# Kernel optimization log

Hardware: AMD Instinct MI355X
Metric: run time of the kernel (lower is better)

The kernel has to match this reference:

```python
import jax, jax.numpy as jnp
import numpy as np
import math

NUM_HEADS = 8
D_HEAD = 128
DEPTH = 1
LAMBDA_INIT = 0.8 - 0.6 * math.exp(-0.3 * DEPTH)
EPS = 1e-5


def setup_inputs() -> dict:
    key = jax.random.key(0)
    ks = jax.random.split(key, 10)
    B, N, D = 2, 2048, 1024
    s = 0.02
    return {
        "X": jax.random.normal(ks[0], (B, N, D), jnp.float32),
        "Wq": jax.random.normal(ks[1], (2 * D_HEAD * NUM_HEADS, D), jnp.float32) * s,
        "Wk": jax.random.normal(ks[2], (2 * D_HEAD * NUM_HEADS, D), jnp.float32) * s,
        "Wv": jax.random.normal(ks[3], (2 * D_HEAD * NUM_HEADS, D), jnp.float32) * s,
        "Wo": jax.random.normal(ks[4], (D, 2 * D_HEAD * NUM_HEADS), jnp.float32) * s,
        "lambda_q1": jax.random.normal(ks[5], (NUM_HEADS, D_HEAD), jnp.float32) * 0.1,
        "lambda_k1": jax.random.normal(ks[6], (NUM_HEADS, D_HEAD), jnp.float32) * 0.1,
        "lambda_q2": jax.random.normal(ks[7], (NUM_HEADS, D_HEAD), jnp.float32) * 0.1,
        "lambda_k2": jax.random.normal(ks[8], (NUM_HEADS, D_HEAD), jnp.float32) * 0.1,
        "rms_scale": jnp.ones((2 * D_HEAD,), jnp.float32),
    }


def reference(X, Wq, Wk, Wv, Wo, lambda_q1, lambda_k1, lambda_q2, lambda_k2, rms_scale):
    B, N, D = X.shape
    H, dh = NUM_HEADS, D_HEAD

    def proj(W):
        # (B, N, 2*H*dh) -> (B, H, N, 2*dh)
        y = jnp.einsum('bnd,ed->bne', X, W)
        return y.reshape(B, N, H, 2 * dh).transpose(0, 2, 1, 3)

    Q = proj(Wq)
    K = proj(Wk)
    V = proj(Wv)
    Q1, Q2 = Q[..., :dh], Q[..., dh:]
    K1, K2 = K[..., :dh], K[..., dh:]

    lam1 = jnp.exp(jnp.sum(lambda_q1 * lambda_k1, axis=-1))  # (H,)
    lam2 = jnp.exp(jnp.sum(lambda_q2 * lambda_k2, axis=-1))
    lam = (lam1 - lam2 + LAMBDA_INIT)[None, :, None, None]  # (1, H, 1, 1)

    scaling = 1.0 / math.sqrt(dh)
    A1 = jnp.einsum('bhqd,bhkd->bhqk', Q1, K1) * scaling
    A2 = jnp.einsum('bhqd,bhkd->bhqk', Q2, K2) * scaling
    attn = jax.nn.softmax(A1, axis=-1) - lam * jax.nn.softmax(A2, axis=-1)

    O = jnp.einsum('bhqk,bhkd->bhqd', attn, V)  # (B, H, N, 2*dh)
    rms = jnp.sqrt(jnp.mean(O * O, axis=-1, keepdims=True) + EPS)
    O = O / rms * rms_scale
    O = O * (1.0 - LAMBDA_INIT)
    O = O.transpose(0, 2, 1, 3).reshape(B, N, H * 2 * dh)
    return jnp.einsum('bne,de->bnd', O, Wo)
```

## Files before the change

### kernel.cpp

```cpp
#include <hip/hip_runtime.h>
#include <hip/hip_bf16.h>

typedef __bf16 bf16;
typedef __attribute__((ext_vector_type(8))) __bf16 bf16x8;
typedef __attribute__((ext_vector_type(4))) float f32x4;

#define LAMBDA_INIT_F 0.3555090675909693f
#define RMS_EPS 1e-5f
#define QSCALE_F 0.1275174053237f

__device__ __forceinline__ void gl_lds16(const bf16* g, bf16* l) {
  __builtin_amdgcn_global_load_lds(
      (const __attribute__((address_space(1))) unsigned int*)g,
      (__attribute__((address_space(3))) unsigned int*)l, 16, 0, 0);
}
__device__ __forceinline__ void gl_lds4(const bf16* g, bf16* l) {
  __builtin_amdgcn_global_load_lds(
      (const __attribute__((address_space(1))) unsigned int*)g,
      (__attribute__((address_space(3))) unsigned int*)l, 4, 0, 0);
}

__global__ void fused_cast(const float* __restrict__ X, const float* __restrict__ Wq,
                           const float* __restrict__ Wk, const float* __restrict__ Wv,
                           const float* __restrict__ Wo, bf16* __restrict__ out) {
  constexpr int T4 = 3145728;
  int idx = blockIdx.x * blockDim.x + threadIdx.x;
  int stride = gridDim.x * blockDim.x;
  for (int i = idx; i < T4; i += stride) {
    const float* src;
    int off;
    if (i < 1048576)       { src = X;  off = i; }
    else if (i < 1572864)  { src = Wq; off = i - 1048576; }
    else if (i < 2097152)  { src = Wk; off = i - 1572864; }
    else if (i < 2621440)  { src = Wv; off = i - 2097152; }
    else                   { src = Wo; off = i - 2621440; }
    float4 v = reinterpret_cast<const float4*>(src)[off];
    bf16 o[4];
    o[0] = (bf16)v.x; o[1] = (bf16)v.y; o[2] = (bf16)v.z; o[3] = (bf16)v.w;
    *reinterpret_cast<ushort4*>(&out[(size_t)i * 4]) = *reinterpret_cast<const ushort4*>(o);
  }
}

template <int MODE, int BM>
__global__ __launch_bounds__(256) void gemm_bt(
    const bf16* __restrict__ A, const bf16* __restrict__ B,
    void* __restrict__ Cv, int M, int N, int K) {
  constexpr int BN = 128, BK = 32;
  constexpr int MF = BM / 32;
  constexpr int CA = BM / 16;
  __shared__ __align__(16) bf16 As[2][BM * BK];
  __shared__ __align__(16) bf16 Bs[2][BN * BK];
  const int tid = threadIdx.x, lane = tid & 63, w = tid >> 6;
  const int l15 = lane & 15, lhi = lane >> 4;
  const int wr = (w >> 1) * (BM / 2), wc = (w & 1) * 64;
  const int bm = blockIdx.x * BM, bn = blockIdx.y * BN;
  const int srow = lane >> 2, scol = (lane & 3) * 8;
  const int NTK = K / BK;
  f32x4 acc[MF][4] = {};

  auto stage = [&](int buf, int k0) {
#pragma unroll
    for (int i = 0; i < CA / 4; ++i) {
      int c = w * (CA / 4) + i;
      gl_lds16(&A[(size_t)(bm + c * 16 + srow) * K + k0 + scol], &As[buf][c * 512]);
    }
#pragma unroll
    for (int i = 0; i < 2; ++i) {
      int c = w * 2 + i;
      gl_lds16(&B[(size_t)(bn + c * 16 + srow) * K + k0 + scol], &Bs[buf][c * 512]);
    }
  };

  stage(0, 0);
  __syncthreads();
  for (int t = 0; t < NTK; ++t) {
    const int buf = t & 1;
    if (t + 1 < NTK) stage(buf ^ 1, (t + 1) * BK);
    bf16x8 af[MF], bfr[4];
#pragma unroll
    for (int mf = 0; mf < MF; ++mf)
      af[mf] = *reinterpret_cast<const bf16x8*>(&As[buf][(wr + mf * 16 + l15) * BK + lhi * 8]);
#pragma unroll
    for (int nf = 0; nf < 4; ++nf)
      bfr[nf] = *reinterpret_cast<const bf16x8*>(&Bs[buf][(wc + nf * 16 + l15) * BK + lhi * 8]);
#pragma unroll
    for (int mf = 0; mf < MF; ++mf)
#pragma unroll
      for (int nf = 0; nf < 4; ++nf)
        acc[mf][nf] = __builtin_amdgcn_mfma_f32_16x16x32_bf16(af[mf], bfr[nf], acc[mf][nf], 0, 0, 0);
    __syncthreads();
  }

#pragma unroll
  for (int mf = 0; mf < MF; ++mf)
#pragma unroll
    for (int nf = 0; nf < 4; ++nf)
#pragma unroll
      for (int r = 0; r < 4; ++r) {
        int m = bm + wr + mf * 16 + lhi * 4 + r;
        int n = bn + wc + nf * 16 + l15;
        if constexpr (MODE == 1) {
          ((float*)Cv)[(size_t)m * N + n] = acc[mf][nf][r];
        } else {
          int reg = n >> 11, nl = n & 2047;
          if (reg == 0) {
            ((bf16*)Cv)[(size_t)m * 2048 + nl] = (bf16)(acc[mf][nf][r] * QSCALE_F);
          } else if (reg == 1) {
            ((bf16*)Cv)[(size_t)(m + 4096) * 2048 + nl] = (bf16)acc[mf][nf][r];
          } else {
            int bb = m >> 11, nq = m & 2047;
            int hh = nl >> 8, e = nl & 255;
            ((bf16*)Cv)[(size_t)16777216 + ((((size_t)bb * 8 + hh) * 256 + e) << 11) + nq] =
                (bf16)acc[mf][nf][r];
          }
        }
      }
}

__global__ __launch_bounds__(512, 4) void diff_attn(
    const bf16* __restrict__ Q, const bf16* __restrict__ Kb, const bf16* __restrict__ Vtg,
    const float* __restrict__ lq1, const float* __restrict__ lk1,
    const float* __restrict__ lq2, const float* __restrict__ lk2,
    const float* __restrict__ rms_scale, bf16* __restrict__ Ob) {
  constexpr int NSEQ = 2048, E = 2048, KT = 32, NT = NSEQ / KT;
  __shared__ __align__(16) char smem[65536];
  float* Z = (float*)smem;

  const int tid = threadIdx.x, lane = tid & 63, w = tid >> 6;
  const int l15 = lane & 15, lhi = lane >> 4;
  const int g = w >> 1, s = w & 1;

  const int bid = blockIdx.x;
  const int orig = (bid & 7) * 64 + (bid >> 3);
  const int bh = orig >> 5;
  const int qb = orig & 31;
  const int b = bh >> 3, h = bh & 7;
  const int q0 = qb * 64;

  float lam = 0.f;
  if (s) {
    float sl1 = 0.f, sl2 = 0.f;
    for (int i = 0; i < 128; ++i) {
      sl1 += lq1[h * 128 + i] * lk1[h * 128 + i];
      sl2 += lq2[h * 128 + i] * lk2[h * 128 + i];
    }
    lam = __expf(sl1) - __expf(sl2) + LAMBDA_INIT_F;
  }

  const size_t qbase = ((size_t)b * NSEQ + q0 + g * 16 + l15) * E + (size_t)h * 256 + s * 128;
  bf16x8 qf[4];
#pragma unroll
  for (int df = 0; df < 4; ++df)
    qf[df] = *reinterpret_cast<const bf16x8*>(&Q[qbase + df * 32 + lhi * 8]);

  const bf16* Kbase = Kb + ((size_t)b * NSEQ) * E + (size_t)h * 256;
  const bf16* Vbase = Vtg + (((size_t)b * 8 + h) * 256) * (size_t)NSEQ;

  const int krow_sub = lane >> 5;
  const int kslot = lane & 31;
  const int ve_sub = lane >> 4;
  const int swz = l15 & 7;
  const int vq2 = (l15 >> 1) & 3;
  const int voff = (lhi ^ vq2) << 3;

  f32x4 o[16] = {};
  float ll = 0.f;

  auto stage = [&](int buf, int t) {
    const int kt0 = t * KT;
    bf16* Ksl = (bf16*)(smem + buf * 32768);
    bf16* Vsl = Ksl + 8192;
#pragma unroll
    for (int i = 0; i < 2; ++i) {
      int c = w * 2 + i;
      int row = 2 * c + krow_sub;
      gl_lds16(&Kbase[(size_t)(kt0 + row) * E + ((kslot ^ (row & 7)) << 3)], &Ksl[c * 512]);
    }
#pragma unroll
    for (int i = 0; i < 8; ++i) {
      int c = w * 8 + i;
      int r = 4 * c + ve_sub;
      int p = (lane & 15) ^ (((r >> 1) & 3) << 2);
      int key0 = 16 * ((p >> 1) & 1) + 4 * (p >> 2) + (p & 1) * 2;
      gl_lds4(&Vbase[(size_t)r * NSEQ + kt0 + key0], &Vsl[c * 128]);
    }
  };

  stage(0, 0);
  __syncthreads();

  for (int t = 0; t < NT; ++t) {
    const int buf = t & 1;
    const bf16* Ksl = (const bf16*)(smem + buf * 32768);
    const bf16* Vsl = Ksl + 8192;

    f32x4 sv0 = {}, sv1 = {};
#pragma unroll
    for (int df = 0; df < 4; ++df) {
      const int slot = (((s << 4) + df * 4 + lhi) ^ swz) << 3;
      bf16x8 kf0 = *reinterpret_cast<const bf16x8*>(&Ksl[l15 * 256 + slot]);
      bf16x8 kf1 = *reinterpret_cast<const bf16x8*>(&Ksl[(16 + l15) * 256 + slot]);
      sv0 = __builtin_amdgcn_mfma_f32_16x16x32_bf16(kf0, qf[df], sv0, 0, 0, 0);
      sv1 = __builtin_amdgcn_mfma_f32_16x16x32_bf16(kf1, qf[df], sv1, 0, 0, 0);
    }

    __builtin_amdgcn_sched_barrier(0);
    if (t + 1 < NT) stage(buf ^ 1, t + 1);
    __builtin_amdgcn_sched_barrier(0);

    bf16 pb[8];
    float rsum = 0.f;
#pragma unroll
    for (int r = 0; r < 4; ++r) {
      float e0 = __builtin_amdgcn_exp2f(sv0[r]);
      float e1 = __builtin_amdgcn_exp2f(sv1[r]);
      rsum += e0 + e1;
      pb[r] = (bf16)e0;
      pb[4 + r] = (bf16)e1;
    }
    ll += rsum;
    bf16x8 pa = *reinterpret_cast<const bf16x8*>(pb);

    __builtin_amdgcn_s_setprio(1);
#pragma unroll
    for (int eb = 0; eb < 16; ++eb) {
      bf16x8 vf = *reinterpret_cast<const bf16x8*>(&Vsl[(eb * 16 + l15) * 32 + voff]);
      o[eb] = __builtin_amdgcn_mfma_f32_16x16x32_bf16(pa, vf, o[eb], 0, 0, 0);
    }
    __builtin_amdgcn_s_setprio(0);

    __syncthreads();
  }

  ll += __shfl_xor(ll, 16, 64);
  ll += __shfl_xor(ll, 32, 64);
  float L[4];
#pragma unroll
  for (int r = 0; r < 4; ++r) L[r] = __shfl(ll, 4 * lhi + r, 64);

  if (s) {
    float* Zg = Z + g * 4096;
#pragma unroll
    for (int r = 0; r < 4; ++r) {
      float i2 = lam / L[r];
#pragma unroll
      for (int eb = 0; eb < 16; ++eb)
        Zg[(4 * lhi + r) * 256 + eb * 16 + l15] = o[eb][r] * i2;
    }
  }
  __syncthreads();
  if (!s) {
    const float osc = 1.0f - LAMBDA_INIT_F;
    const float* Zg = Z + g * 4096;
#pragma unroll
    for (int r = 0; r < 4; ++r) {
      float i1 = 1.0f / L[r];
      float vals[16];
      float ssq = 0.f;
#pragma unroll
      for (int eb = 0; eb < 16; ++eb) {
        float v = o[eb][r] * i1 - Zg[(4 * lhi + r) * 256 + eb * 16 + l15];
        vals[eb] = v;
        ssq += v * v;
      }
#pragma unroll
      for (int off = 1; off < 16; off <<= 1) ssq += __shfl_xor(ssq, off, 64);
      float rinv = rsqrtf(ssq * (1.0f / 256.0f) + RMS_EPS);
      const int q = q0 + g * 16 + 4 * lhi + r;
      const size_t ob = ((size_t)b * NSEQ + q) * E + (size_t)h * 256;
#pragma unroll
      for (int eb = 0; eb < 16; ++eb) {
        int e = eb * 16 + l15;
        Ob[ob + e] = (bf16)(vals[eb] * rinv * rms_scale[e] * osc);
      }
    }
  }
}

extern "C" void kernel_launch(void* const* d_in, const int* in_sizes, int n_in,
                              void* d_out, int out_size, void* d_ws, size_t ws_size,
                              hipStream_t stream) {
  const float* X   = (const float*)d_in[0];
  const float* Wq  = (const float*)d_in[1];
  const float* Wk  = (const float*)d_in[2];
  const float* Wv  = (const float*)d_in[3];
  const float* Wo  = (const float*)d_in[4];
  const float* lq1 = (const float*)d_in[5];
  const float* lk1 = (const float*)d_in[6];
  const float* lq2 = (const float*)d_in[7];
  const float* lk2 = (const float*)d_in[8];
  const float* rs  = (const float*)d_in[9];
  float* out = (float*)d_out;

  constexpr size_t B = 2, NSEQ = 2048, D = 1024, E = 2048;
  constexpr size_t M = B * NSEQ;

  char* ws = (char*)d_ws;
  bf16* Xb  = (bf16*)ws;
  bf16* Wqb = Xb + M * D;
  bf16* Wkb = Wqb + E * D;
  bf16* Wvb = Wkb + E * D;
  bf16* Wob = Wvb + E * D;
  bf16* Qb  = Wob + D * E;
  bf16* Kb  = Qb + M * E;
  bf16* Vtb = Kb + M * E;
  bf16* Ob  = Vtb + M * E;

  fused_cast<<<2048, 256, 0, stream>>>(X, Wq, Wk, Wv, Wo, Xb);

  gemm_bt<3, 128><<<dim3(M / 128, 6144 / 128), 256, 0, stream>>>(
      Xb, Wqb, Qb, (int)M, 6144, (int)D);

  diff_attn<<<dim3(512), 512, 0, stream>>>(Qb, Kb, Vtb, lq1, lk1, lq2, lk2, rs, Ob);

  gemm_bt<1, 64><<<dim3(M / 64, D / 128), 256, 0, stream>>>(Ob, Wob, out, (int)M, (int)D, (int)E);
}
```

Before: 275.3 us.

## Switch differential attention to 32x32x16 MFMA tiles with 128-query blocks

Rewrites the attention kernel around 32x32x16 bf16 MFMA instead of 16x16x32. Each block now covers 128 queries, so the grid halves and each K/V tile loaded into LDS is reused across more queries. V is now staged with 16-byte global-to-LDS loads, with K and V staging split across different waves. Probabilities are packed with v_cvt_pk_bf16_f32 and exchanged across lanes to form the operand, and the cross-wave Z buffer is stored as bf16. The rms_scale and output-scale multiply moves into the Wo bf16 cast. Costs and risks: register pressure is higher (launch bounds drop to 2 waves), there is extra shuffle work, and Z loses precision.

```diff
diff --git a/kernel.cpp b/kernel.cpp
--- a/kernel.cpp
+++ b/kernel.cpp
@@ -4,6 +4,8 @@
 typedef __bf16 bf16;
 typedef __attribute__((ext_vector_type(8))) __bf16 bf16x8;
 typedef __attribute__((ext_vector_type(4))) float f32x4;
+typedef __attribute__((ext_vector_type(16))) float f32x16;
+typedef __attribute__((ext_vector_type(4))) unsigned int u32x4;
 
 #define LAMBDA_INIT_F 0.3555090675909693f
 #define RMS_EPS 1e-5f
@@ -14,27 +16,30 @@
       (const __attribute__((address_space(1))) unsigned int*)g,
       (__attribute__((address_space(3))) unsigned int*)l, 16, 0, 0);
 }
-__device__ __forceinline__ void gl_lds4(const bf16* g, bf16* l) {
-  __builtin_amdgcn_global_load_lds(
-      (const __attribute__((address_space(1))) unsigned int*)g,
-      (__attribute__((address_space(3))) unsigned int*)l, 4, 0, 0);
-}
 
 __global__ void fused_cast(const float* __restrict__ X, const float* __restrict__ Wq,
                            const float* __restrict__ Wk, const float* __restrict__ Wv,
-                           const float* __restrict__ Wo, bf16* __restrict__ out) {
+                           const float* __restrict__ Wo, const float* __restrict__ rs,
+                           bf16* __restrict__ out) {
   constexpr int T4 = 3145728;
+  constexpr float OSC = 1.0f - LAMBDA_INIT_F;
   int idx = blockIdx.x * blockDim.x + threadIdx.x;
   int stride = gridDim.x * blockDim.x;
   for (int i = idx; i < T4; i += stride) {
     const float* src;
     int off;
+    bool isWo = false;
     if (i < 1048576)       { src = X;  off = i; }
     else if (i < 1572864)  { src = Wq; off = i - 1048576; }
     else if (i < 2097152)  { src = Wk; off = i - 1572864; }
     else if (i < 2621440)  { src = Wv; off = i - 2097152; }
-    else                   { src = Wo; off = i - 2621440; }
+    else                   { src = Wo; off = i - 2621440; isWo = true; }
     float4 v = reinterpret_cast<const float4*>(src)[off];
+    if (isWo) {
+      int r0 = (off * 4) & 255;
+      v.x *= rs[r0] * OSC; v.y *= rs[r0 + 1] * OSC;
+      v.z *= rs[r0 + 2] * OSC; v.w *= rs[r0 + 3] * OSC;
+    }
     bf16 o[4];
     o[0] = (bf16)v.x; o[1] = (bf16)v.y; o[2] = (bf16)v.z; o[3] = (bf16)v.w;
     *reinterpret_cast<ushort4*>(&out[(size_t)i * 4]) = *reinterpret_cast<const ushort4*>(o);
@@ -117,25 +122,22 @@
       }
 }
 
-__global__ __launch_bounds__(512, 4) void diff_attn(
+__global__ __launch_bounds__(512, 2) void diff_attn(
     const bf16* __restrict__ Q, const bf16* __restrict__ Kb, const bf16* __restrict__ Vtg,
     const float* __restrict__ lq1, const float* __restrict__ lk1,
     const float* __restrict__ lq2, const float* __restrict__ lk2,
-    const float* __restrict__ rms_scale, bf16* __restrict__ Ob) {
+    bf16* __restrict__ Ob) {
   constexpr int NSEQ = 2048, E = 2048, KT = 32, NT = NSEQ / KT;
   __shared__ __align__(16) char smem[65536];
-  float* Z = (float*)smem;
-
   const int tid = threadIdx.x, lane = tid & 63, w = tid >> 6;
-  const int l15 = lane & 15, lhi = lane >> 4;
+  const int q = lane & 31, hi = lane >> 5;
   const int g = w >> 1, s = w & 1;
 
   const int bid = blockIdx.x;
-  const int orig = (bid & 7) * 64 + (bid >> 3);
-  const int bh = orig >> 5;
-  const int qb = orig & 31;
+  const int orig = (bid & 7) * 32 + (bid >> 3);
+  const int bh = orig >> 4, qb = orig & 15;
   const int b = bh >> 3, h = bh & 7;
-  const int q0 = qb * 64;
+  const int q0 = qb * 128;
 
   float lam = 0.f;
   if (s) {
@@ -147,42 +149,39 @@
     lam = __expf(sl1) - __expf(sl2) + LAMBDA_INIT_F;
   }
 
-  const size_t qbase = ((size_t)b * NSEQ + q0 + g * 16 + l15) * E + (size_t)h * 256 + s * 128;
-  bf16x8 qf[4];
-#pragma unroll
-  for (int df = 0; df < 4; ++df)
-    qf[df] = *reinterpret_cast<const bf16x8*>(&Q[qbase + df * 32 + lhi * 8]);
-
-  const bf16* Kbase = Kb + ((size_t)b * NSEQ) * E + (size_t)h * 256;
-  const bf16* Vbase = Vtg + (((size_t)b * 8 + h) * 256) * (size_t)NSEQ;
-
-  const int krow_sub = lane >> 5;
+  const bf16* Qr = Q + ((size_t)b * NSEQ + q0 + g * 32 + q) * E + h * 256 + s * 128 + hi * 8;
+  bf16x8 qf[8];
+#pragma unroll
+  for (int df = 0; df < 8; ++df)
+    qf[df] = *reinterpret_cast<const bf16x8*>(Qr + df * 16);
+
+  const bf16* Kbase = Kb + (size_t)b * NSEQ * E + h * 256;
+  const bf16* Vbase = Vtg + ((size_t)b * 8 + h) * 256 * (size_t)NSEQ;
+
   const int kslot = lane & 31;
-  const int ve_sub = lane >> 4;
-  const int swz = l15 & 7;
-  const int vq2 = (l15 >> 1) & 3;
-  const int voff = (lhi ^ vq2) << 3;
-
-  f32x4 o[16] = {};
+
+  f32x16 o[8] = {};
   float ll = 0.f;
 
   auto stage = [&](int buf, int t) {
     const int kt0 = t * KT;
     bf16* Ksl = (bf16*)(smem + buf * 32768);
     bf16* Vsl = Ksl + 8192;
-#pragma unroll
-    for (int i = 0; i < 2; ++i) {
-      int c = w * 2 + i;
-      int row = 2 * c + krow_sub;
-      gl_lds16(&Kbase[(size_t)(kt0 + row) * E + ((kslot ^ (row & 7)) << 3)], &Ksl[c * 512]);
-    }
-#pragma unroll
-    for (int i = 0; i < 8; ++i) {
-      int c = w * 8 + i;
-      int r = 4 * c + ve_sub;
-      int p = (lane & 15) ^ (((r >> 1) & 3) << 2);
-      int key0 = 16 * ((p >> 1) & 1) + 4 * (p >> 2) + (p & 1) * 2;
-      gl_lds4(&Vbase[(size_t)r * NSEQ + kt0 + key0], &Vsl[c * 128]);
+    if (w < 4) {
+#pragma unroll
+      for (int i = 0; i < 4; ++i) {
+        int c = w * 4 + i;
+        int row = 2 * c + hi;
+        gl_lds16(&Kbase[(size_t)(kt0 + row) * E + ((kslot ^ (row & 7)) << 3)], &Ksl[c * 512]);
+      }
+    } else {
+#pragma unroll
+      for (int i = 0; i < 4; ++i) {
+        int c = (w - 4) * 4 + i;
+        int erow = (c >> 1) * 32 + q;
+        int koff = (c & 1) * 16 + hi * 8;
+        gl_lds16(&Vbase[(size_t)erow * NSEQ + kt0 + koff], &Vsl[c * 512]);
+      }
     }
   };
 
@@ -194,86 +193,117 @@
     const bf16* Ksl = (const bf16*)(smem + buf * 32768);
     const bf16* Vsl = Ksl + 8192;
 
-    f32x4 sv0 = {}, sv1 = {};
-#pragma unroll
-    for (int df = 0; df < 4; ++df) {
-      const int slot = (((s << 4) + df * 4 + lhi) ^ swz) << 3;
-      bf16x8 kf0 = *reinterpret_cast<const bf16x8*>(&Ksl[l15 * 256 + slot]);
-      bf16x8 kf1 = *reinterpret_cast<const bf16x8*>(&Ksl[(16 + l15) * 256 + slot]);
-      sv0 = __builtin_amdgcn_mfma_f32_16x16x32_bf16(kf0, qf[df], sv0, 0, 0, 0);
-      sv1 = __builtin_amdgcn_mfma_f32_16x16x32_bf16(kf1, qf[df], sv1, 0, 0, 0);
+    f32x16 sv0 = {}, sv1 = {};
+#pragma unroll
+    for (int df = 0; df < 8; df += 2) {
+      int sl0 = ((s * 16 + df * 2 + hi) ^ (q & 7)) << 3;
+      bf16x8 kf0 = *reinterpret_cast<const bf16x8*>(&Ksl[q * 256 + sl0]);
+      sv0 = __builtin_amdgcn_mfma_f32_32x32x16_bf16(kf0, qf[df], sv0, 0, 0, 0);
+      int sl1 = ((s * 16 + (df + 1) * 2 + hi) ^ (q & 7)) << 3;
+      bf16x8 kf1 = *reinterpret_cast<const bf16x8*>(&Ksl[q * 256 + sl1]);
+      sv1 = __builtin_amdgcn_mfma_f32_32x32x16_bf16(kf1, qf[df + 1], sv1, 0, 0, 0);
     }
 
     __builtin_amdgcn_sched_barrier(0);
     if (t + 1 < NT) stage(buf ^ 1, t + 1);
     __builtin_amdgcn_sched_barrier(0);
 
-    bf16 pb[8];
-    float rsum = 0.f;
-#pragma unroll
-    for (int r = 0; r < 4; ++r) {
-      float e0 = __builtin_amdgcn_exp2f(sv0[r]);
-      float e1 = __builtin_amdgcn_exp2f(sv1[r]);
-      rsum += e0 + e1;
-      pb[r] = (bf16)e0;
-      pb[4 + r] = (bf16)e1;
-    }
-    ll += rsum;
-    bf16x8 pa = *reinterpret_cast<const bf16x8*>(pb);
+    float p[16];
+#pragma unroll
+    for (int r = 0; r < 16; ++r) {
+      p[r] = __builtin_amdgcn_exp2f(sv0[r] + sv1[r]);
+      ll += p[r];
+    }
+
+    unsigned int pkw[8], pw[8];
+#pragma unroll
+    for (int jj = 0; jj < 8; ++jj) {
+      unsigned int u;
+      asm("v_cvt_pk_bf16_f32 %0, %1, %2" : "=v"(u) : "v"(p[2 * jj]), "v"(p[2 * jj + 1]));
+      pkw[jj] = u;
+    }
+#pragma unroll
+    for (int jj = 0; jj < 8; ++jj)
+      pw[jj] = (unsigned int)__shfl_xor((int)pkw[jj], 32, 64);
+
+    u32x4 f0, f1;
+    f0[0] = hi ? pw[2] : pkw[0];
+    f0[1] = hi ? pw[3] : pkw[1];
+    f0[2] = hi ? pkw[2] : pw[0];
+    f0[3] = hi ? pkw[3] : pw[1];
+    f1[0] = hi ? pw[6] : pkw[4];
+    f1[1] = hi ? pw[7] : pkw[5];
+    f1[2] = hi ? pkw[6] : pw[4];
+    f1[3] = hi ? pkw[7] : pw[5];
+    bf16x8 pb0 = __builtin_bit_cast(bf16x8, f0);
+    bf16x8 pb1 = __builtin_bit_cast(bf16x8, f1);
 
     __builtin_amdgcn_s_setprio(1);
 #pragma unroll
-    for (int eb = 0; eb < 16; ++eb) {
-      bf16x8 vf = *reinterpret_cast<const bf16x8*>(&Vsl[(eb * 16 + l15) * 32 + voff]);
-      o[eb] = __builtin_amdgcn_mfma_f32_16x16x32_bf16(pa, vf, o[eb], 0, 0, 0);
+    for (int eb = 0; eb < 8; ++eb) {
+      bf16x8 va = *reinterpret_cast<const bf16x8*>(&Vsl[(eb * 2) * 512 + lane * 8]);
+      o[eb] = __builtin_amdgcn_mfma_f32_32x32x16_bf16(va, pb0, o[eb], 0, 0, 0);
+      bf16x8 vb = *reinterpret_cast<const bf16x8*>(&Vsl[(eb * 2 + 1) * 512 + lane * 8]);
+      o[eb] = __builtin_amdgcn_mfma_f32_32x32x16_bf16(vb, pb1, o[eb], 0, 0, 0);
     }
     __builtin_amdgcn_s_setprio(0);
 
     __syncthreads();
   }
 
-  ll += __shfl_xor(ll, 16, 64);
   ll += __shfl_xor(ll, 32, 64);
-  float L[4];
-#pragma unroll
-  for (int r = 0; r < 4; ++r) L[r] = __shfl(ll, 4 * lhi + r, 64);
+  unsigned int* Zg = (unsigned int*)smem + g * 4096;
 
   if (s) {
-    float* Zg = Z + g * 4096;
-#pragma unroll
-    for (int r = 0; r < 4; ++r) {
-      float i2 = lam / L[r];
-#pragma unroll
-      for (int eb = 0; eb < 16; ++eb)
-        Zg[(4 * lhi + r) * 256 + eb * 16 + l15] = o[eb][r] * i2;
-    }
+    float i2 = lam / ll;
+#pragma unroll
+    for (int eb = 0; eb < 8; ++eb)
+#pragma unroll
+      for (int j = 0; j < 8; ++j) {
+        int r0 = 2 * j;
+        int crow0 = (r0 & 3) + 8 * (r0 >> 2) + 4 * hi;
+        int e2 = eb * 16 + (crow0 >> 1);
+        float z0 = o[eb][2 * j] * i2, z1 = o[eb][2 * j + 1] * i2;
+        unsigned int u;
+        asm("v_cvt_pk_bf16_f32 %0, %1, %2" : "=v"(u) : "v"(z0), "v"(z1));
+        Zg[e2 * 32 + q] = u;
+      }
   }
   __syncthreads();
   if (!s) {
-    const float osc = 1.0f - LAMBDA_INIT_F;
-    const float* Zg = Z + g * 4096;
-#pragma unroll
-    for (int r = 0; r < 4; ++r) {
-      float i1 = 1.0f / L[r];
-      float vals[16];
-      float ssq = 0.f;
-#pragma unroll
-      for (int eb = 0; eb < 16; ++eb) {
-        float v = o[eb][r] * i1 - Zg[(4 * lhi + r) * 256 + eb * 16 + l15];
-        vals[eb] = v;
-        ssq += v * v;
-      }
-#pragma unroll
-      for (int off = 1; off < 16; off <<= 1) ssq += __shfl_xor(ssq, off, 64);
-      float rinv = rsqrtf(ssq * (1.0f / 256.0f) + RMS_EPS);
-      const int q = q0 + g * 16 + 4 * lhi + r;
-      const size_t ob = ((size_t)b * NSEQ + q) * E + (size_t)h * 256;
-#pragma unroll
-      for (int eb = 0; eb < 16; ++eb) {
-        int e = eb * 16 + l15;
-        Ob[ob + e] = (bf16)(vals[eb] * rinv * rms_scale[e] * osc);
-      }
-    }
+    float i1 = 1.0f / ll;
+    float ssq = 0.f;
+#pragma unroll
+    for (int eb = 0; eb < 8; ++eb)
+#pragma unroll
+      for (int j = 0; j < 8; ++j) {
+        int r0 = 2 * j;
+        int crow0 = (r0 & 3) + 8 * (r0 >> 2) + 4 * hi;
+        int e2 = eb * 16 + (crow0 >> 1);
+        unsigned int u = Zg[e2 * 32 + q];
+        float z0 = __uint_as_float(u << 16);
+        float z1 = __uint_as_float(u & 0xffff0000u);
+        float v0 = o[eb][2 * j] * i1 - z0;
+        float v1 = o[eb][2 * j + 1] * i1 - z1;
+        o[eb][2 * j] = v0;
+        o[eb][2 * j + 1] = v1;
+        ssq += v0 * v0 + v1 * v1;
+      }
+    ssq += __shfl_xor(ssq, 32, 64);
+    float rinv = rsqrtf(ssq * (1.0f / 256.0f) + RMS_EPS);
+    unsigned int* Og = (unsigned int*)Ob;
+    const size_t orow = ((size_t)b * NSEQ + q0 + g * 32 + q) * E + h * 256;
+#pragma unroll
+    for (int eb = 0; eb < 8; ++eb)
+#pragma unroll
+      for (int j = 0; j < 8; ++j) {
+        int r0 = 2 * j;
+        int crow0 = (r0 & 3) + 8 * (r0 >> 2) + 4 * hi;
+        float v0 = o[eb][2 * j] * rinv, v1 = o[eb][2 * j + 1] * rinv;
+        unsigned int u;
+        asm("v_cvt_pk_bf16_f32 %0, %1, %2" : "=v"(u) : "v"(v0), "v"(v1));
+        Og[(orow + eb * 32 + crow0) >> 1] = u;
+      }
   }
 }
 
@@ -306,12 +336,12 @@
   bf16* Vtb = Kb + M * E;
   bf16* Ob  = Vtb + M * E;
 
-  fused_cast<<<2048, 256, 0, stream>>>(X, Wq, Wk, Wv, Wo, Xb);
+  fused_cast<<<2048, 256, 0, stream>>>(X, Wq, Wk, Wv, Wo, rs, Xb);
 
   gemm_bt<3, 128><<<dim3(M / 128, 6144 / 128), 256, 0, stream>>>(
       Xb, Wqb, Qb, (int)M, 6144, (int)D);
 
-  diff_attn<<<dim3(512), 512, 0, stream>>>(Qb, Kb, Vtb, lq1, lk1, lq2, lk2, rs, Ob);
+  diff_attn<<<dim3(256), 512, 0, stream>>>(Qb, Kb, Vtb, lq1, lk1, lq2, lk2, Ob);
 
   gemm_bt<1, 64><<<dim3(M / 64, D / 128), 256, 0, stream>>>(Ob, Wob, out, (int)M, (int)D, (int)E);
 }
```

Result: faster. 250.6 us (-9.0%).
